# Performance work log

Hardware: AMD Instinct MI355X
Metric: run time of the kernel (lower is better)

Reference implementation:

```python
import jax, jax.numpy as jnp
import numpy as np

QMIN, QMAX = -128, 127


def setup_inputs() -> dict:
    key = jax.random.key(0)
    kx, kw, kb = jax.random.split(key, 3)
    B, S, IN, OUT = 4, 2048, 4096, 4096
    x = jax.random.normal(kx, (B, S, IN), dtype=jnp.float32)
    # int8-valued weight stored as int32 for portability
    weight_int = jax.random.randint(kw, (OUT, IN), QMIN, QMAX + 1, dtype=jnp.int32)
    bias = jax.random.normal(kb, (OUT,), dtype=jnp.float32) * 0.02
    # plausible frozen qparams: x~N(0,1) -> range ~[-4,4]; weight range ~[-3,3] pre-quant
    scale_a = jnp.asarray(8.0 / 255.0, dtype=jnp.float32)
    zp_a = jnp.asarray(0, dtype=jnp.int32)
    weight_scale = jnp.asarray(6.0 / 255.0, dtype=jnp.float32)
    weight_zero_point = jnp.asarray(0, dtype=jnp.int32)
    return {
        "x": x,
        "weight_int": weight_int,
        "bias": bias,
        "scale_a": scale_a,
        "zp_a": zp_a,
        "weight_scale": weight_scale,
        "weight_zero_point": weight_zero_point,
    }


def reference(x, weight_int, bias, scale_a, zp_a, weight_scale, weight_zero_point):
    # fake-quantize activations: round(x/scale)+zp, clamp to int8 range
    zp_a_f = zp_a.astype(jnp.float32)
    x_int8 = jnp.clip(jnp.round(x / scale_a) + zp_a_f, QMIN, QMAX)
    x_cent = x_int8 - zp_a_f                                   # [B,S,IN]
    w_cent = weight_int.astype(jnp.float32) - weight_zero_point.astype(jnp.float32)  # [OUT,IN]
    y = jnp.einsum("bsi,oi->bso", x_cent, w_cent)              # dequant-space GEMM
    y = y * (scale_a * weight_scale)
    y = y + bias
    return y
```

## Files before the change

### kernel.cpp

```cpp
#include <hip/hip_runtime.h>
#include <stdint.h>

typedef int v4i  __attribute__((ext_vector_type(4)));
typedef int v16i __attribute__((ext_vector_type(16)));

__global__ void quant_x_kernel(const float* __restrict__ x,
                               int8_t* __restrict__ xq,
                               int* __restrict__ sum_x,
                               const float* __restrict__ p_scale,
                               const int* __restrict__ p_zp,
                               int K) {
    const int row = blockIdx.x;
    const int t = threadIdx.x;
    const float s = p_scale[0];
    const float zpf = (float)p_zp[0];
    const float* xr = x + (size_t)row * K;
    int8_t* qr = xq + (size_t)row * K;
    int lsum = 0;
    const int nchunk = K >> 10;
    for (int i = 0; i < nchunk; ++i) {
        const int idx = (i << 10) + (t << 2);
        const float4 v = *reinterpret_cast<const float4*>(xr + idx);
        const float f0 = fminf(fmaxf(rintf(v.x / s) + zpf, -128.f), 127.f);
        const float f1 = fminf(fmaxf(rintf(v.y / s) + zpf, -128.f), 127.f);
        const float f2 = fminf(fmaxf(rintf(v.z / s) + zpf, -128.f), 127.f);
        const float f3 = fminf(fmaxf(rintf(v.w / s) + zpf, -128.f), 127.f);
        const int i0 = (int)f0, i1 = (int)f1, i2 = (int)f2, i3 = (int)f3;
        lsum += i0 + i1 + i2 + i3;
        const unsigned pk = (unsigned)(i0 & 255) | ((unsigned)(i1 & 255) << 8) |
                            ((unsigned)(i2 & 255) << 16) | ((unsigned)(i3 & 255) << 24);
        *reinterpret_cast<unsigned*>(qr + idx) = pk;
    }
    __shared__ int wsum[4];
    #pragma unroll
    for (int off = 32; off > 0; off >>= 1) lsum += __shfl_down(lsum, off);
    if ((t & 63) == 0) wsum[t >> 6] = lsum;
    __syncthreads();
    if (t == 0) sum_x[row] = wsum[0] + wsum[1] + wsum[2] + wsum[3];
}

__global__ void quant_w_kernel(const int* __restrict__ w,
                               int8_t* __restrict__ wq,
                               int* __restrict__ sum_w,
                               int K) {
    const int row = blockIdx.x;
    const int t = threadIdx.x;
    const int* wr_ = w + (size_t)row * K;
    int8_t* qr = wq + (size_t)row * K;
    int lsum = 0;
    const int nchunk = K >> 10;
    for (int i = 0; i < nchunk; ++i) {
        const int idx = (i << 10) + (t << 2);
        const int4 v = *reinterpret_cast<const int4*>(wr_ + idx);
        lsum += v.x + v.y + v.z + v.w;
        const unsigned pk = (unsigned)(v.x & 255) | ((unsigned)(v.y & 255) << 8) |
                            ((unsigned)(v.z & 255) << 16) | ((unsigned)(v.w & 255) << 24);
        *reinterpret_cast<unsigned*>(qr + idx) = pk;
    }
    __shared__ int wsum[4];
    #pragma unroll
    for (int off = 32; off > 0; off >>= 1) lsum += __shfl_down(lsum, off);
    if ((t & 63) == 0) wsum[t >> 6] = lsum;
    __syncthreads();
    if (t == 0) sum_w[row] = wsum[0] + wsum[1] + wsum[2] + wsum[3];
}

#define BM 256
#define BN 256
#define BKB 64
#define NSLOT 4

__device__ __forceinline__ void gload_lds16(const void* g, void* l) {
    __builtin_amdgcn_global_load_lds(
        (const __attribute__((address_space(1))) unsigned int*)g,
        (__attribute__((address_space(3))) unsigned int*)l, 16, 0, 0);
}

#define MFMA_I8 __builtin_amdgcn_mfma_i32_32x32x32_i8

__global__ __launch_bounds__(512, 2)
void gemm_i8_kernel(const int8_t* __restrict__ xq,
                    const int8_t* __restrict__ wq,
                    const int* __restrict__ sum_x,
                    const int* __restrict__ sum_w,
                    const float* __restrict__ bias,
                    float* __restrict__ out,
                    const float* __restrict__ p_sa,
                    const int* __restrict__ p_zpa,
                    const float* __restrict__ p_sw,
                    const int* __restrict__ p_wzp,
                    int M, int N, int K) {
    __shared__ v4i ldsA[NSLOT][1024];
    __shared__ v4i ldsB[NSLOT][1024];

    const int tid = threadIdx.x;
    const int lane = tid & 63;
    const int wid = tid >> 6;
    const int wr = wid >> 2;
    const int wc = wid & 3;
    const int m0 = blockIdx.y * BM;
    const int n0 = blockIdx.x * BN;

    const int srow = tid >> 2;
    const int schunk = (tid & 3) ^ (((srow >> 1) ^ (srow >> 3)) & 3);
    const int8_t* aS = xq + (size_t)(m0 + srow) * K + schunk * 16;
    const int8_t* bS = wq + (size_t)(n0 + srow) * K + schunk * 16;
    const size_t half = (size_t)128 * K;
    const int dbase = wid * 64;

    const int sel = ((lane >> 1) ^ (lane >> 3)) & 3;
    const int hi = lane >> 5;
    const int abase = (wr * 128 + (lane & 31)) * 4;
    const int bbase = (wc * 64 + (lane & 31)) * 4;
    const int c00 = hi ^ sel;
    const int c01 = (2 + hi) ^ sel;

    v16i acc[4][2] = {};
    const int NT = K / BKB;

    gload_lds16(aS,             &ldsA[0][dbase]);
    gload_lds16(aS + half,      &ldsA[0][dbase + 512]);
    gload_lds16(bS,             &ldsB[0][dbase]);
    gload_lds16(bS + half,      &ldsB[0][dbase + 512]);
    gload_lds16(aS + 64,        &ldsA[1][dbase]);
    gload_lds16(aS + half + 64, &ldsA[1][dbase + 512]);
    gload_lds16(bS + 64,        &ldsB[1][dbase]);
    gload_lds16(bS + half + 64, &ldsB[1][dbase + 512]);
    asm volatile("s_waitcnt vmcnt(4)" ::: "memory");
    __builtin_amdgcn_sched_barrier(0);
    __builtin_amdgcn_s_barrier();

    for (int t = 0; t < NT; ++t) {
        const v4i* LA = ldsA[t & 3];
        const v4i* LB = ldsB[t & 3];

        const v4i b00 = LB[bbase + c00];
        const v4i b01 = LB[bbase + c01];
        const v4i b10 = LB[bbase + 128 + c00];
        const v4i b11 = LB[bbase + 128 + c01];
        const v4i a00 = LA[abase + c00];
        const v4i a01 = LA[abase + c01];
        const v4i a10 = LA[abase + 128 + c00];
        const v4i a11 = LA[abase + 128 + c01];
        if (t + 2 < NT) {
            const int ns = (t + 2) & 3;
            const int8_t* p = aS + (size_t)(t + 2) * BKB;
            gload_lds16(p,        &ldsA[ns][dbase]);
            gload_lds16(p + half, &ldsA[ns][dbase + 512]);
        }
        __builtin_amdgcn_s_barrier();
        __builtin_amdgcn_s_setprio(1);
        acc[0][0] = MFMA_I8(a00, b00, acc[0][0], 0, 0, 0);
        acc[0][1] = MFMA_I8(a00, b10, acc[0][1], 0, 0, 0);
        acc[1][0] = MFMA_I8(a10, b00, acc[1][0], 0, 0, 0);
        acc[1][1] = MFMA_I8(a10, b10, acc[1][1], 0, 0, 0);
        acc[0][0] = MFMA_I8(a01, b01, acc[0][0], 0, 0, 0);
        acc[0][1] = MFMA_I8(a01, b11, acc[0][1], 0, 0, 0);
        acc[1][0] = MFMA_I8(a11, b01, acc[1][0], 0, 0, 0);
        acc[1][1] = MFMA_I8(a11, b11, acc[1][1], 0, 0, 0);
        __builtin_amdgcn_s_setprio(0);
        __builtin_amdgcn_s_barrier();

        const v4i a20 = LA[abase + 256 + c00];
        const v4i a21 = LA[abase + 256 + c01];
        const v4i a30 = LA[abase + 384 + c00];
        const v4i a31 = LA[abase + 384 + c01];
        if (t + 2 < NT) {
            const int ns = (t + 2) & 3;
            const int8_t* p = bS + (size_t)(t + 2) * BKB;
            gload_lds16(p,        &ldsB[ns][dbase]);
            gload_lds16(p + half, &ldsB[ns][dbase + 512]);
        }
        __builtin_amdgcn_s_barrier();
        __builtin_amdgcn_s_setprio(1);
        acc[2][0] = MFMA_I8(a20, b00, acc[2][0], 0, 0, 0);
        acc[2][1] = MFMA_I8(a20, b10, acc[2][1], 0, 0, 0);
        acc[3][0] = MFMA_I8(a30, b00, acc[3][0], 0, 0, 0);
        acc[3][1] = MFMA_I8(a30, b10, acc[3][1], 0, 0, 0);
        acc[2][0] = MFMA_I8(a21, b01, acc[2][0], 0, 0, 0);
        acc[2][1] = MFMA_I8(a21, b11, acc[2][1], 0, 0, 0);
        acc[3][0] = MFMA_I8(a31, b01, acc[3][0], 0, 0, 0);
        acc[3][1] = MFMA_I8(a31, b11, acc[3][1], 0, 0, 0);
        __builtin_amdgcn_s_setprio(0);
        if (t + 2 < NT) {
            asm volatile("s_waitcnt vmcnt(4)" ::: "memory");
        } else if (t + 1 < NT) {
            asm volatile("s_waitcnt vmcnt(0)" ::: "memory");
        }
        __builtin_amdgcn_sched_barrier(0);
        __builtin_amdgcn_s_barrier();
    }

    const float stot = p_sa[0] * p_sw[0];
    const int zpa = p_zpa[0];
    const int wzp = p_wzp[0];
    const int kzz = K * zpa * wzp;
    const int coll = lane & 31;
    const int rhi = (lane >> 5) * 4;

    #pragma unroll
    for (int cf = 0; cf < 2; ++cf) {
        const int cg = n0 + wc * 64 + cf * 32 + coll;
        const int sw = sum_w[cg];
        const float bb = bias[cg];
        #pragma unroll
        for (int rf = 0; rf < 4; ++rf) {
            const int rbase = m0 + wr * 128 + rf * 32 + rhi;
            #pragma unroll
            for (int r = 0; r < 16; ++r) {
                const int rowg = rbase + (r & 3) + 8 * (r >> 2);
                const int iv = acc[rf][cf][r] - wzp * sum_x[rowg] - zpa * sw + kzz;
                out[(size_t)rowg * N + cg] = (float)iv * stot + bb;
            }
        }
    }
}

extern "C" void kernel_launch(void* const* d_in, const int* in_sizes, int n_in,
                              void* d_out, int out_size, void* d_ws, size_t ws_size,
                              hipStream_t stream) {
    const float* x     = (const float*)d_in[0];
    const int*   w     = (const int*)d_in[1];
    const float* bias  = (const float*)d_in[2];
    const float* p_sa  = (const float*)d_in[3];
    const int*   p_zpa = (const int*)d_in[4];
    const float* p_sw  = (const float*)d_in[5];
    const int*   p_wzp = (const int*)d_in[6];

    const int N = in_sizes[2];
    const int K = in_sizes[1] / N;
    const int M = in_sizes[0] / K;

    int8_t* xq = (int8_t*)d_ws;
    int8_t* wq = xq + (size_t)M * K;
    int* sum_x = (int*)(wq + (size_t)N * K);
    int* sum_w = sum_x + M;

    quant_x_kernel<<<M, 256, 0, stream>>>(x, xq, sum_x, p_sa, p_zpa, K);
    quant_w_kernel<<<N, 256, 0, stream>>>(w, wq, sum_w, K);

    dim3 grid(N / BN, M / BM);
    gemm_i8_kernel<<<grid, 512, 0, stream>>>(xq, wq, sum_x, sum_w, bias,
                                             (float*)d_out, p_sa, p_zpa, p_sw, p_wzp,
                                             M, N, K);
}
```

Measured before the change: 239.1 us.

## Use 4 waves with 128x128 per-wave tiles and XCD-aware block remapping

The GEMM block shrinks from 8 waves to 4, so each wave now computes a 128x128 output tile (4x4 MFMA accumulators) instead of 128x64. The two half-iteration phases with intermediate barriers are merged into one phase per k-step with a single combined staging macro. A 1D grid with a modulo-8 remap spreads blocks across XCDs to improve L2 locality. The trade-off is more accumulator registers (256 VGPRs of accumulators) and fewer waves to hide latency, at one block per CU.

```diff
diff --git a/kernel.cpp b/kernel.cpp
--- a/kernel.cpp
+++ b/kernel.cpp
@@ -78,7 +78,7 @@
 
 #define MFMA_I8 __builtin_amdgcn_mfma_i32_32x32x32_i8
 
-__global__ __launch_bounds__(512, 2)
+__global__ __launch_bounds__(256, 1)
 void gemm_i8_kernel(const int8_t* __restrict__ xq,
                     const int8_t* __restrict__ wq,
                     const int* __restrict__ sum_x,
@@ -96,100 +96,86 @@
     const int tid = threadIdx.x;
     const int lane = tid & 63;
     const int wid = tid >> 6;
-    const int wr = wid >> 2;
-    const int wc = wid & 3;
-    const int m0 = blockIdx.y * BM;
-    const int n0 = blockIdx.x * BN;
+    const int wr = wid >> 1;
+    const int wc = wid & 1;
+
+    const int nwgy = M / BM;
+    const int nwg = nwgy * (N / BN);
+    const int bid = blockIdx.x;
+    const int v = (bid & 7) * (nwg >> 3) + (bid >> 3);
+    const int m0 = (v % nwgy) * BM;
+    const int n0 = (v / nwgy) * BN;
 
     const int srow = tid >> 2;
     const int schunk = (tid & 3) ^ (((srow >> 1) ^ (srow >> 3)) & 3);
     const int8_t* aS = xq + (size_t)(m0 + srow) * K + schunk * 16;
     const int8_t* bS = wq + (size_t)(n0 + srow) * K + schunk * 16;
-    const size_t half = (size_t)128 * K;
+    const size_t qtr = (size_t)64 * K;
     const int dbase = wid * 64;
 
     const int sel = ((lane >> 1) ^ (lane >> 3)) & 3;
     const int hi = lane >> 5;
-    const int abase = (wr * 128 + (lane & 31)) * 4;
-    const int bbase = (wc * 64 + (lane & 31)) * 4;
-    const int c00 = hi ^ sel;
-    const int c01 = (2 + hi) ^ sel;
-
-    v16i acc[4][2] = {};
+    const int c0 = hi ^ sel;
+    const int c1 = (2 + hi) ^ sel;
+    int arow[4], brow[4];
+    #pragma unroll
+    for (int i = 0; i < 4; ++i) {
+        arow[i] = (wr * 128 + i * 32 + (lane & 31)) * 4;
+        brow[i] = (wc * 128 + i * 32 + (lane & 31)) * 4;
+    }
+
+    v16i acc[4][4] = {};
     const int NT = K / BKB;
 
-    gload_lds16(aS,             &ldsA[0][dbase]);
-    gload_lds16(aS + half,      &ldsA[0][dbase + 512]);
-    gload_lds16(bS,             &ldsB[0][dbase]);
-    gload_lds16(bS + half,      &ldsB[0][dbase + 512]);
-    gload_lds16(aS + 64,        &ldsA[1][dbase]);
-    gload_lds16(aS + half + 64, &ldsA[1][dbase + 512]);
-    gload_lds16(bS + 64,        &ldsB[1][dbase]);
-    gload_lds16(bS + half + 64, &ldsB[1][dbase + 512]);
-    asm volatile("s_waitcnt vmcnt(4)" ::: "memory");
+#define STAGE(SLOT, T_) do {                                                  \
+        const int8_t* pa_ = aS + (size_t)(T_) * BKB;                          \
+        const int8_t* pb_ = bS + (size_t)(T_) * BKB;                          \
+        _Pragma("unroll")                                                     \
+        for (int k_ = 0; k_ < 4; ++k_) {                                      \
+            gload_lds16(pa_ + k_ * qtr, &ldsA[SLOT][k_ * 256 + dbase]);       \
+            gload_lds16(pb_ + k_ * qtr, &ldsB[SLOT][k_ * 256 + dbase]);       \
+        }                                                                     \
+    } while (0)
+
+    STAGE(0, 0);
+    STAGE(1, 1);
+    asm volatile("s_waitcnt vmcnt(8)" ::: "memory");
     __builtin_amdgcn_sched_barrier(0);
     __builtin_amdgcn_s_barrier();
 
     for (int t = 0; t < NT; ++t) {
         const v4i* LA = ldsA[t & 3];
         const v4i* LB = ldsB[t & 3];
-
-        const v4i b00 = LB[bbase + c00];
-        const v4i b01 = LB[bbase + c01];
-        const v4i b10 = LB[bbase + 128 + c00];
-        const v4i b11 = LB[bbase + 128 + c01];
-        const v4i a00 = LA[abase + c00];
-        const v4i a01 = LA[abase + c01];
-        const v4i a10 = LA[abase + 128 + c00];
-        const v4i a11 = LA[abase + 128 + c01];
-        if (t + 2 < NT) {
-            const int ns = (t + 2) & 3;
-            const int8_t* p = aS + (size_t)(t + 2) * BKB;
-            gload_lds16(p,        &ldsA[ns][dbase]);
-            gload_lds16(p + half, &ldsA[ns][dbase + 512]);
-        }
-        __builtin_amdgcn_s_barrier();
+        v4i a[4][2], b[4][2];
+        #pragma unroll
+        for (int i = 0; i < 4; ++i) {
+            a[i][0] = LA[arow[i] + c0];
+            a[i][1] = LA[arow[i] + c1];
+        }
+        #pragma unroll
+        for (int i = 0; i < 4; ++i) {
+            b[i][0] = LB[brow[i] + c0];
+            b[i][1] = LB[brow[i] + c1];
+        }
+        if (t + 2 < NT) STAGE((t + 2) & 3, t + 2);
         __builtin_amdgcn_s_setprio(1);
-        acc[0][0] = MFMA_I8(a00, b00, acc[0][0], 0, 0, 0);
-        acc[0][1] = MFMA_I8(a00, b10, acc[0][1], 0, 0, 0);
-        acc[1][0] = MFMA_I8(a10, b00, acc[1][0], 0, 0, 0);
-        acc[1][1] = MFMA_I8(a10, b10, acc[1][1], 0, 0, 0);
-        acc[0][0] = MFMA_I8(a01, b01, acc[0][0], 0, 0, 0);
-        acc[0][1] = MFMA_I8(a01, b11, acc[0][1], 0, 0, 0);
-        acc[1][0] = MFMA_I8(a11, b01, acc[1][0], 0, 0, 0);
-        acc[1][1] = MFMA_I8(a11, b11, acc[1][1], 0, 0, 0);
-        __builtin_amdgcn_s_setprio(0);
-        __builtin_amdgcn_s_barrier();
-
-        const v4i a20 = LA[abase + 256 + c00];
-        const v4i a21 = LA[abase + 256 + c01];
-        const v4i a30 = LA[abase + 384 + c00];
-        const v4i a31 = LA[abase + 384 + c01];
-        if (t + 2 < NT) {
-            const int ns = (t + 2) & 3;
-            const int8_t* p = bS + (size_t)(t + 2) * BKB;
-            gload_lds16(p,        &ldsB[ns][dbase]);
-            gload_lds16(p + half, &ldsB[ns][dbase + 512]);
-        }
-        __builtin_amdgcn_s_barrier();
-        __builtin_amdgcn_s_setprio(1);
-        acc[2][0] = MFMA_I8(a20, b00, acc[2][0], 0, 0, 0);
-        acc[2][1] = MFMA_I8(a20, b10, acc[2][1], 0, 0, 0);
-        acc[3][0] = MFMA_I8(a30, b00, acc[3][0], 0, 0, 0);
-        acc[3][1] = MFMA_I8(a30, b10, acc[3][1], 0, 0, 0);
-        acc[2][0] = MFMA_I8(a21, b01, acc[2][0], 0, 0, 0);
-        acc[2][1] = MFMA_I8(a21, b11, acc[2][1], 0, 0, 0);
-        acc[3][0] = MFMA_I8(a31, b01, acc[3][0], 0, 0, 0);
-        acc[3][1] = MFMA_I8(a31, b11, acc[3][1], 0, 0, 0);
+        #pragma unroll
+        for (int ks = 0; ks < 2; ++ks)
+            #pragma unroll
+            for (int rf = 0; rf < 4; ++rf)
+                #pragma unroll
+                for (int cf = 0; cf < 4; ++cf)
+                    acc[rf][cf] = MFMA_I8(a[rf][ks], b[cf][ks], acc[rf][cf], 0, 0, 0);
         __builtin_amdgcn_s_setprio(0);
         if (t + 2 < NT) {
-            asm volatile("s_waitcnt vmcnt(4)" ::: "memory");
+            asm volatile("s_waitcnt vmcnt(8)" ::: "memory");
         } else if (t + 1 < NT) {
             asm volatile("s_waitcnt vmcnt(0)" ::: "memory");
         }
         __builtin_amdgcn_sched_barrier(0);
         __builtin_amdgcn_s_barrier();
     }
+#undef STAGE
 
     const float stot = p_sa[0] * p_sw[0];
     const int zpa = p_zpa[0];
@@ -199,8 +185,8 @@
     const int rhi = (lane >> 5) * 4;
 
     #pragma unroll
-    for (int cf = 0; cf < 2; ++cf) {
-        const int cg = n0 + wc * 64 + cf * 32 + coll;
+    for (int cf = 0; cf < 4; ++cf) {
+        const int cg = n0 + wc * 128 + cf * 32 + coll;
         const int sw = sum_w[cg];
         const float bb = bias[cg];
         #pragma unroll
@@ -239,8 +225,8 @@
     quant_x_kernel<<<M, 256, 0, stream>>>(x, xq, sum_x, p_sa, p_zpa, K);
     quant_w_kernel<<<N, 256, 0, stream>>>(w, wq, sum_w, K);
 
-    dim3 grid(N / BN, M / BM);
-    gemm_i8_kernel<<<grid, 512, 0, stream>>>(xq, wq, sum_x, sum_w, bias,
-                                             (float*)d_out, p_sa, p_zpa, p_sw, p_wzp,
-                                             M, N, K);
-}
+    const int nwg = (M / BM) * (N / BN);
+    gemm_i8_kernel<<<nwg, 256, 0, stream>>>(xq, wq, sum_x, sum_w, bias,
+                                            (float*)d_out, p_sa, p_zpa, p_sw, p_wzp,
+                                            M, N, K);
+}
```

After: 238.4 us. About the same (-0.3%).
